# Kernel tuning notes

Measured on AMD Instinct MI355X. Metric: run time of the kernel, lower is better.

The kernel has to match this reference:

```python
import jax, jax.numpy as jnp
import numpy as np

HEAD_NUM = 8
QKV_DIM = 16
EMB = 128
SQRT_EMB = 11.313708498984761  # sqrt(128)
LOGIT_CLIP = 10.0


def _heads(x):
    # (B, n, H*d) -> (B, H, n, d)
    B, n, _ = x.shape
    return x.reshape(B, n, HEAD_NUM, QKV_DIM).transpose(0, 2, 1, 3)


def _mha(q, k, v, rank3_ninf_mask):
    # q: (B,H,n,d), k/v: (B,H,m,d), mask: (B,n,m)
    score = jnp.einsum('bhnd,bhmd->bhnm', q, k) / jnp.sqrt(jnp.float32(QKV_DIM))
    score = score + rank3_ninf_mask[:, None, :, :]
    w = jax.nn.softmax(score, axis=3)
    out = jnp.einsum('bhnm,bhmd->bhnd', w, v)
    B, H, n, d = out.shape
    return out.transpose(0, 2, 1, 3).reshape(B, n, H * d)


def setup_inputs() -> dict:
    key = jax.random.key(0)
    ks = jax.random.split(key, 20)
    B, N, P = 32, 512, 512
    s = 1.0 / np.sqrt(EMB)
    inp = {
        'encoded_nodes': jax.random.normal(ks[0], (B, N, EMB), jnp.float32),
        'encoded_graph': jax.random.normal(ks[1], (B, N, EMB), jnp.float32),
        'encoded_q1': jax.random.normal(ks[2], (B, P, EMB), jnp.float32),
        'encoded_first_graph': jax.random.normal(ks[3], (B, P, EMB), jnp.float32),
        'encoded_last_node': jax.random.normal(ks[4], (B, P, EMB), jnp.float32),
        'encoded_last_graph': jax.random.normal(ks[5], (B, P, EMB), jnp.float32),
        'ninf_mask': jnp.zeros((B, P, N), jnp.float32),
        # weights stored (in, out); torch Linear y = x @ W.T
        'Wq_first': jax.random.uniform(ks[6], (EMB, EMB), jnp.float32, -s, s),
        'Wq_last': jax.random.uniform(ks[7], (EMB, EMB), jnp.float32, -s, s),
        'Wk': jax.random.uniform(ks[8], (EMB, EMB), jnp.float32, -s, s),
        'Wv': jax.random.uniform(ks[9], (EMB, EMB), jnp.float32, -s, s),
        'Wq_first_e': jax.random.uniform(ks[10], (EMB, EMB), jnp.float32, -s, s),
        'Wq_last_e': jax.random.uniform(ks[11], (EMB, EMB), jnp.float32, -s, s),
        'Wk_e': jax.random.uniform(ks[12], (EMB, EMB), jnp.float32, -s, s),
        'Wv_e': jax.random.uniform(ks[13], (EMB, EMB), jnp.float32, -s, s),
        'Wcomb1': jax.random.uniform(ks[14], (EMB, EMB), jnp.float32, -s, s),
        'bcomb1': jax.random.uniform(ks[15], (EMB,), jnp.float32, -s, s),
        'Wcomb2': jax.random.uniform(ks[16], (EMB, EMB), jnp.float32, -s, s),
        'bcomb2': jax.random.uniform(ks[17], (EMB,), jnp.float32, -s, s),
    }
    return inp


def reference(encoded_nodes, encoded_graph, encoded_q1, encoded_first_graph,
              encoded_last_node, encoded_last_graph, ninf_mask,
              Wq_first, Wq_last, Wk, Wv,
              Wq_first_e, Wq_last_e, Wk_e, Wv_e,
              Wcomb1, bcomb1, Wcomb2, bcomb2):
    # set_kv
    k = _heads(encoded_nodes @ Wk)
    v = _heads(encoded_nodes @ Wv)
    k_e = _heads(encoded_graph @ Wk_e)
    v_e = _heads(encoded_graph @ Wv_e)
    # set_q1
    q_first = _heads(encoded_q1 @ Wq_first)
    q_first_e = _heads(encoded_first_graph @ Wq_first_e)
    # forward
    q_last = _heads(encoded_last_node @ Wq_last)
    q_last_e = _heads(encoded_last_graph @ Wq_last_e)
    q = (q_first + q_last) + (q_first_e + q_last_e)
    out1 = _mha(q, k, v, ninf_mask)
    out2 = _mha(q, k_e, v_e, ninf_mask)
    mh_out = (out1 @ Wcomb1 + bcomb1) + (out2 @ Wcomb2 + bcomb2)
    # single-head scoring against summed keys: (B,n,e) x (B,N,e) -> (B,n,N)
    shk = encoded_nodes + encoded_graph
    score = jnp.einsum('bne,bNe->bnN', mh_out, shk) / SQRT_EMB
    score = LOGIT_CLIP * jnp.tanh(score) + ninf_mask
    probs = jax.nn.softmax(score, axis=2)
    return probs
```

## Files before the change

### kernel.cpp

```cpp
#include <hip/hip_runtime.h>

#define BATCH 32
#define SEQ   512
#define EMBD  128
#define HEADS 8
#define HD    16
#define ROWS  (BATCH*SEQ)
#define TILE_R 64
#define NTILES (ROWS/TILE_R)

__device__ __forceinline__ void gemm_tile(const float* __restrict__ A,
                                          const float* __restrict__ W,
                                          int rowBase, int tid,
                                          float* sA, float* sW,
                                          float acc[8][4])
{
    __syncthreads();
    {
        const float4* Ag = (const float4*)(A + (size_t)rowBase * EMBD);
        const float4* Wg = (const float4*)W;
        float4* sA4 = (float4*)sA;
        float4* sW4 = (float4*)sW;
        #pragma unroll
        for (int k = 0; k < 8; ++k)  sA4[tid + k*256] = Ag[tid + k*256];
        #pragma unroll
        for (int k = 0; k < 16; ++k) sW4[tid + k*256] = Wg[tid + k*256];
    }
    __syncthreads();
    const int r0 = (tid >> 5) * 8;
    const int c0 = (tid & 31) * 4;
    for (int e0 = 0; e0 < EMBD; e0 += 4) {
        float a[8][4];
        #pragma unroll
        for (int r = 0; r < 8; ++r)
            *(float4*)&a[r][0] = *(const float4*)&sA[(r0+r)*EMBD + e0];
        float w[4][4];
        #pragma unroll
        for (int j = 0; j < 4; ++j)
            *(float4*)&w[j][0] = *(const float4*)&sW[(e0+j)*EMBD + c0];
        #pragma unroll
        for (int r = 0; r < 8; ++r) {
            #pragma unroll
            for (int c = 0; c < 4; ++c)
                acc[r][c] += a[r][0]*w[0][c] + a[r][1]*w[1][c]
                           + a[r][2]*w[2][c] + a[r][3]*w[3][c];
        }
    }
}

__device__ __forceinline__ void store_tile(float* __restrict__ out,
                                           int rowBase, int tid,
                                           float acc[8][4])
{
    const int r0 = (tid >> 5) * 8;
    const int c0 = (tid & 31) * 4;
    #pragma unroll
    for (int r = 0; r < 8; ++r)
        *(float4*)(out + (size_t)(rowBase + r0 + r)*EMBD + c0) =
            make_float4(acc[r][0], acc[r][1], acc[r][2], acc[r][3]);
}

__global__ __launch_bounds__(256) void proj_q_kernel(
    const float* __restrict__ A0, const float* __restrict__ W0,
    const float* __restrict__ A1, const float* __restrict__ W1,
    const float* __restrict__ A2, const float* __restrict__ W2,
    const float* __restrict__ A3, const float* __restrict__ W3,
    float* __restrict__ out)
{
    extern __shared__ float smem[];
    float* sA = smem;
    float* sW = smem + TILE_R*EMBD;
    const int tid = threadIdx.x;
    const int rowBase = blockIdx.x * TILE_R;
    float acc[8][4];
    #pragma unroll
    for (int r = 0; r < 8; ++r)
        #pragma unroll
        for (int c = 0; c < 4; ++c) acc[r][c] = 0.f;
    gemm_tile(A0, W0, rowBase, tid, sA, sW, acc);
    gemm_tile(A1, W1, rowBase, tid, sA, sW, acc);
    gemm_tile(A2, W2, rowBase, tid, sA, sW, acc);
    gemm_tile(A3, W3, rowBase, tid, sA, sW, acc);
    store_tile(out, rowBase, tid, acc);
}

__global__ __launch_bounds__(256) void proj_kv_kernel(
    const float* __restrict__ nodes, const float* __restrict__ graph,
    const float* __restrict__ Wk,  const float* __restrict__ Wv,
    const float* __restrict__ Wke, const float* __restrict__ Wve,
    float* __restrict__ Kb, float* __restrict__ Vb,
    float* __restrict__ Keb, float* __restrict__ Veb)
{
    extern __shared__ float smem[];
    float* sA = smem;
    float* sW = smem + TILE_R*EMBD;
    const int tid = threadIdx.x;
    const int rowBase = blockIdx.x * TILE_R;
    const int job = blockIdx.y;
    const float* A = (job < 2) ? nodes : graph;
    const float* W = (job == 0) ? Wk : (job == 1) ? Wv : (job == 2) ? Wke : Wve;
    float* out    = (job == 0) ? Kb : (job == 1) ? Vb : (job == 2) ? Keb : Veb;
    float acc[8][4];
    #pragma unroll
    for (int r = 0; r < 8; ++r)
        #pragma unroll
        for (int c = 0; c < 4; ++c) acc[r][c] = 0.f;
    gemm_tile(A, W, rowBase, tid, sA, sW, acc);
    store_tile(out, rowBase, tid, acc);
}

__global__ __launch_bounds__(256) void combine_kernel(
    const float* __restrict__ A0, const float* __restrict__ W0,
    const float* __restrict__ A1, const float* __restrict__ W1,
    const float* __restrict__ b0, const float* __restrict__ b1,
    float* __restrict__ out)
{
    extern __shared__ float smem[];
    float* sA = smem;
    float* sW = smem + TILE_R*EMBD;
    const int tid = threadIdx.x;
    const int rowBase = blockIdx.x * TILE_R;
    const int c0 = (tid & 31) * 4;
    float bv[4];
    #pragma unroll
    for (int c = 0; c < 4; ++c) bv[c] = b0[c0+c] + b1[c0+c];
    float acc[8][4];
    #pragma unroll
    for (int r = 0; r < 8; ++r)
        #pragma unroll
        for (int c = 0; c < 4; ++c) acc[r][c] = bv[c];
    gemm_tile(A0, W0, rowBase, tid, sA, sW, acc);
    gemm_tile(A1, W1, rowBase, tid, sA, sW, acc);
    store_tile(out, rowBase, tid, acc);
}

__global__ __launch_bounds__(512) void attn_kernel(
    const float* __restrict__ Qm, const float* __restrict__ Km,
    const float* __restrict__ Vm, const float* __restrict__ Kem,
    const float* __restrict__ Vem, const float* __restrict__ mask,
    float* __restrict__ out1, float* __restrict__ out2)
{
    extern __shared__ float smem[];
    float4* sK  = (float4*)smem;
    float4* sV  = sK  + 2048;
    float4* sKe = sV  + 2048;
    float4* sVe = sKe + 2048;
    const int tid = threadIdx.x;
    const int b = blockIdx.x >> 3;
    const int h = blockIdx.x & 7;
    const int base4 = b*(SEQ*EMBD/4) + h*(HD/4);
    {
        const float4* K4  = (const float4*)Km;
        const float4* V4  = (const float4*)Vm;
        const float4* Ke4 = (const float4*)Kem;
        const float4* Ve4 = (const float4*)Vem;
        #pragma unroll
        for (int k = 0; k < 4; ++k) {
            int i = tid + k*512;
            int m = i >> 2, j = i & 3;
            int g = base4 + m*(EMBD/4) + j;
            sK[i]  = K4[g];
            sV[i]  = V4[g];
            sKe[i] = Ke4[g];
            sVe[i] = Ve4[g];
        }
    }
    __syncthreads();

    const int row = tid;
    float q[16];
    {
        const float4* Q4 = (const float4*)Qm;
        #pragma unroll
        for (int j = 0; j < 4; ++j)
            *(float4*)&q[j*4] = Q4[base4 + row*(EMBD/4) + j];
    }
    const float* mrow = mask + ((size_t)b*SEQ + row)*SEQ;

    float l1 = 0.f, l2 = 0.f;
    float acc1[16], acc2[16];
    #pragma unroll
    for (int d = 0; d < 16; ++d) { acc1[d] = 0.f; acc2[d] = 0.f; }

    for (int m = 0; m < SEQ; ++m) {
        const float mk = mrow[m];
        {
            float4 k0 = sK[m*4+0], k1 = sK[m*4+1], k2 = sK[m*4+2], k3 = sK[m*4+3];
            float s = q[0]*k0.x + q[1]*k0.y + q[2]*k0.z + q[3]*k0.w
                    + q[4]*k1.x + q[5]*k1.y + q[6]*k1.z + q[7]*k1.w
                    + q[8]*k2.x + q[9]*k2.y + q[10]*k2.z + q[11]*k2.w
                    + q[12]*k3.x + q[13]*k3.y + q[14]*k3.z + q[15]*k3.w;
            float p = __expf(s*0.25f + mk);
            l1 += p;
            float4 v0 = sV[m*4+0], v1 = sV[m*4+1], v2 = sV[m*4+2], v3 = sV[m*4+3];
            acc1[0]+=p*v0.x;  acc1[1]+=p*v0.y;  acc1[2]+=p*v0.z;  acc1[3]+=p*v0.w;
            acc1[4]+=p*v1.x;  acc1[5]+=p*v1.y;  acc1[6]+=p*v1.z;  acc1[7]+=p*v1.w;
            acc1[8]+=p*v2.x;  acc1[9]+=p*v2.y;  acc1[10]+=p*v2.z; acc1[11]+=p*v2.w;
            acc1[12]+=p*v3.x; acc1[13]+=p*v3.y; acc1[14]+=p*v3.z; acc1[15]+=p*v3.w;
        }
        {
            float4 k0 = sKe[m*4+0], k1 = sKe[m*4+1], k2 = sKe[m*4+2], k3 = sKe[m*4+3];
            float s = q[0]*k0.x + q[1]*k0.y + q[2]*k0.z + q[3]*k0.w
                    + q[4]*k1.x + q[5]*k1.y + q[6]*k1.z + q[7]*k1.w
                    + q[8]*k2.x + q[9]*k2.y + q[10]*k2.z + q[11]*k2.w
                    + q[12]*k3.x + q[13]*k3.y + q[14]*k3.z + q[15]*k3.w;
            float p = __expf(s*0.25f + mk);
            l2 += p;
            float4 v0 = sVe[m*4+0], v1 = sVe[m*4+1], v2 = sVe[m*4+2], v3 = sVe[m*4+3];
            acc2[0]+=p*v0.x;  acc2[1]+=p*v0.y;  acc2[2]+=p*v0.z;  acc2[3]+=p*v0.w;
            acc2[4]+=p*v1.x;  acc2[5]+=p*v1.y;  acc2[6]+=p*v1.z;  acc2[7]+=p*v1.w;
            acc2[8]+=p*v2.x;  acc2[9]+=p*v2.y;  acc2[10]+=p*v2.z; acc2[11]+=p*v2.w;
            acc2[12]+=p*v3.x; acc2[13]+=p*v3.y; acc2[14]+=p*v3.z; acc2[15]+=p*v3.w;
        }
    }
    const float inv1 = 1.f / l1;
    const float inv2 = 1.f / l2;
    float4* o14 = (float4*)out1;
    float4* o24 = (float4*)out2;
    #pragma unroll
    for (int j = 0; j < 4; ++j) {
        o14[base4 + row*(EMBD/4) + j] = make_float4(acc1[j*4]*inv1, acc1[j*4+1]*inv1,
                                                    acc1[j*4+2]*inv1, acc1[j*4+3]*inv1);
        o24[base4 + row*(EMBD/4) + j] = make_float4(acc2[j*4]*inv2, acc2[j*4+1]*inv2,
                                                    acc2[j*4+2]*inv2, acc2[j*4+3]*inv2);
    }
}

#define RB 16
#define MT 128
__global__ __launch_bounds__(256) void final_kernel(
    const float* __restrict__ mh, const float* __restrict__ nodes,
    const float* __restrict__ graph, const float* __restrict__ mask,
    float* __restrict__ out)
{
    extern __shared__ float smem[];
    float*  sShk = smem;
    float*  sMh  = smem + MT*EMBD;
    float*  sS   = sMh + RB*EMBD;
    float*  sInv = sS + RB*SEQ;
    float4* sShk4 = (float4*)sShk;
    const int tid  = threadIdx.x;
    const int b    = blockIdx.x >> 5;
    const int row0 = (blockIdx.x & 31) * RB;

    {
        const float4* mh4 = (const float4*)(mh + ((size_t)b*SEQ + row0)*EMBD);
        ((float4*)sMh)[tid]       = mh4[tid];
        ((float4*)sMh)[tid + 256] = mh4[tid + 256];
    }

    const int mg = tid & 63;
    const int rg = tid >> 6;
    const float4* n4 = (const float4*)nodes;
    const float4* g4 = (const float4*)graph;

    for (int mt = 0; mt < SEQ/MT; ++mt) {
        const int m0 = mt * MT;
        __syncthreads();
        {
            const int gb = (b*SEQ + m0) * (EMBD/4);
            #pragma unroll
            for (int k = 0; k < 16; ++k) {
                int i = tid + k*256;
                int m = i >> 5, f = i & 31;
                float4 x = n4[gb + m*32 + f];
                float4 y = g4[gb + m*32 + f];
                float4 s4;
                s4.x = x.x + y.x; s4.y = x.y + y.y;
                s4.z = x.z + y.z; s4.w = x.w + y.w;
                sShk4[(m << 5) | (f ^ (m & 31))] = s4;
            }
        }
        __syncthreads();

        float acc[4][2];
        #pragma unroll
        for (int r = 0; r < 4; ++r) { acc[r][0] = 0.f; acc[r][1] = 0.f; }
        const int mA = mg*2, mB = mg*2 + 1;
        for (int e0 = 0; e0 < EMBD; e0 += 4) {
            const int f = e0 >> 2;
            float a[4][4];
            #pragma unroll
            for (int r = 0; r < 4; ++r)
                *(float4*)&a[r][0] = *(const float4*)&sMh[(rg*4+r)*EMBD + e0];
            float s0[4], s1[4];
            *(float4*)&s0[0] = sShk4[(mA << 5) | (f ^ (mA & 31))];
            *(float4*)&s1[0] = sShk4[(mB << 5) | (f ^ (mB & 31))];
            #pragma unroll
            for (int r = 0; r < 4; ++r) {
                acc[r][0] += a[r][0]*s0[0] + a[r][1]*s0[1] + a[r][2]*s0[2] + a[r][3]*s0[3];
                acc[r][1] += a[r][0]*s1[0] + a[r][1]*s1[1] + a[r][2]*s1[2] + a[r][3]*s1[3];
            }
        }
        #pragma unroll
        for (int r = 0; r < 4; ++r) {
            const int rr = rg*4 + r;
            const size_t mbase = ((size_t)b*SEQ + row0 + rr) * SEQ;
            #pragma unroll
            for (int mm = 0; mm < 2; ++mm) {
                const int m = m0 + mg*2 + mm;
                float sc = 10.f * tanhf(acc[r][mm] * 0.088388347648318447f)
                         + mask[mbase + m];
                sS[rr*SEQ + m] = sc;
            }
        }
    }
    __syncthreads();

    {
        const int r = tid >> 4, g = tid & 15;
        float sum = 0.f;
        for (int k = g; k < SEQ; k += 16) {
            float p = __expf(sS[r*SEQ + k]);
            sS[r*SEQ + k] = p;
            sum += p;
        }
        #pragma unroll
        for (int off = 8; off >= 1; off >>= 1) sum += __shfl_xor(sum, off, 16);
        if (g == 0) sInv[r] = 1.f / sum;
    }
    __syncthreads();

    float* orow = out + ((size_t)b*SEQ + row0) * SEQ;
    #pragma unroll
    for (int k = 0; k < 32; ++k) {
        int i = tid + k*256;
        int r = i >> 9;
        orow[i] = sS[i] * sInv[r];
    }
}

extern "C" void kernel_launch(void* const* d_in, const int* in_sizes, int n_in,
                              void* d_out, int out_size, void* d_ws, size_t ws_size,
                              hipStream_t stream)
{
    const float* nodes = (const float*)d_in[0];
    const float* graph = (const float*)d_in[1];
    const float* q1    = (const float*)d_in[2];
    const float* fg    = (const float*)d_in[3];
    const float* ln    = (const float*)d_in[4];
    const float* lg    = (const float*)d_in[5];
    const float* mask  = (const float*)d_in[6];
    const float* Wqf   = (const float*)d_in[7];
    const float* Wql   = (const float*)d_in[8];
    const float* Wk    = (const float*)d_in[9];
    const float* Wv    = (const float*)d_in[10];
    const float* Wqfe  = (const float*)d_in[11];
    const float* Wqle  = (const float*)d_in[12];
    const float* Wke   = (const float*)d_in[13];
    const float* Wve   = (const float*)d_in[14];
    const float* Wc1   = (const float*)d_in[15];
    const float* bc1   = (const float*)d_in[16];
    const float* Wc2   = (const float*)d_in[17];
    const float* bc2   = (const float*)d_in[18];

    float* ws = (float*)d_ws;
    const size_t BUF = (size_t)ROWS * EMBD;
    float* Qb  = ws;
    float* Kb  = ws + BUF;
    float* Vb  = ws + 2*BUF;
    float* Keb = ws + 3*BUF;
    float* Veb = ws + 4*BUF;
    float* mhb = Qb;
    float* o1  = (float*)d_out;
    float* o2  = o1 + BUF;

    const int LDS_GEMM  = (TILE_R*EMBD + EMBD*EMBD) * 4;
    const int LDS_ATTN  = 4 * SEQ * HD * 4;
    const int LDS_FINAL = (MT*EMBD + RB*EMBD + RB*SEQ + 16) * 4;
    hipFuncSetAttribute((const void*)proj_q_kernel,  hipFuncAttributeMaxDynamicSharedMemorySize, LDS_GEMM);
    hipFuncSetAttribute((const void*)proj_kv_kernel, hipFuncAttributeMaxDynamicSharedMemorySize, LDS_GEMM);
    hipFuncSetAttribute((const void*)combine_kernel, hipFuncAttributeMaxDynamicSharedMemorySize, LDS_GEMM);
    hipFuncSetAttribute((const void*)attn_kernel,    hipFuncAttributeMaxDynamicSharedMemorySize, LDS_ATTN);
    hipFuncSetAttribute((const void*)final_kernel,   hipFuncAttributeMaxDynamicSharedMemorySize, LDS_FINAL);

    proj_q_kernel<<<NTILES, 256, LDS_GEMM, stream>>>(
        q1, Wqf, ln, Wql, fg, Wqfe, lg, Wqle, Qb);
    proj_kv_kernel<<<dim3(NTILES, 4), 256, LDS_GEMM, stream>>>(
        nodes, graph, Wk, Wv, Wke, Wve, Kb, Vb, Keb, Veb);
    attn_kernel<<<BATCH*HEADS, 512, LDS_ATTN, stream>>>(
        Qb, Kb, Vb, Keb, Veb, mask, o1, o2);
    combine_kernel<<<NTILES, 256, LDS_GEMM, stream>>>(
        o1, Wc1, o2, Wc2, bc1, bc2, mhb);
    final_kernel<<<BATCH*32, 256, LDS_FINAL, stream>>>(
        mhb, nodes, graph, mask, (float*)d_out);
}
```

Baseline: 683.4 us.

## Drop LDS from projection GEMMs, merge projections, re-split attention and final softmax

Merges the Q and KV projection launches into one kernel and makes the projection and combine GEMMs read operands straight from global/cache instead of staging them in LDS, using smaller 32-row tiles. The attention kernel is reorganised so each 1024-thread block handles two heads of one K/V type instead of one head with both types, with vectorised mask loads. The final kernel keeps probabilities in registers with a wave-level row reduction instead of an LDS score buffer, and computes tanh through exp. The aim is more parallelism and fewer LDS round-trips and barriers, at the cost of more redundant global reads of weights and activations.

After: 653.3 us. 1.05x faster.

```diff
diff --git a/kernel.cpp b/kernel.cpp
--- a/kernel.cpp
+++ b/kernel.cpp
@@ -6,107 +6,86 @@
 #define HEADS 8
 #define HD    16
 #define ROWS  (BATCH*SEQ)
-#define TILE_R 64
-#define NTILES (ROWS/TILE_R)
-
-__device__ __forceinline__ void gemm_tile(const float* __restrict__ A,
-                                          const float* __restrict__ W,
-                                          int rowBase, int tid,
-                                          float* sA, float* sW,
-                                          float acc[8][4])
-{
-    __syncthreads();
-    {
-        const float4* Ag = (const float4*)(A + (size_t)rowBase * EMBD);
-        const float4* Wg = (const float4*)W;
-        float4* sA4 = (float4*)sA;
-        float4* sW4 = (float4*)sW;
-        #pragma unroll
-        for (int k = 0; k < 8; ++k)  sA4[tid + k*256] = Ag[tid + k*256];
-        #pragma unroll
-        for (int k = 0; k < 16; ++k) sW4[tid + k*256] = Wg[tid + k*256];
-    }
-    __syncthreads();
-    const int r0 = (tid >> 5) * 8;
+#define GR    32
+#define NT32  (ROWS/GR)
+
+__device__ __forceinline__ void gemm_nolds(const float* __restrict__ A,
+                                           const float* __restrict__ W,
+                                           int rowBase, int tid,
+                                           float acc[4][4])
+{
+    const int r0 = (tid >> 5) * 4;
     const int c0 = (tid & 31) * 4;
+    const float* Ab = A + (size_t)(rowBase + r0) * EMBD;
     for (int e0 = 0; e0 < EMBD; e0 += 4) {
-        float a[8][4];
-        #pragma unroll
-        for (int r = 0; r < 8; ++r)
-            *(float4*)&a[r][0] = *(const float4*)&sA[(r0+r)*EMBD + e0];
-        float w[4][4];
+        float4 a[4];
+        #pragma unroll
+        for (int r = 0; r < 4; ++r)
+            a[r] = *(const float4*)(Ab + r*EMBD + e0);
+        float4 w[4];
         #pragma unroll
         for (int j = 0; j < 4; ++j)
-            *(float4*)&w[j][0] = *(const float4*)&sW[(e0+j)*EMBD + c0];
-        #pragma unroll
-        for (int r = 0; r < 8; ++r) {
-            #pragma unroll
-            for (int c = 0; c < 4; ++c)
-                acc[r][c] += a[r][0]*w[0][c] + a[r][1]*w[1][c]
-                           + a[r][2]*w[2][c] + a[r][3]*w[3][c];
-        }
-    }
-}
-
-__device__ __forceinline__ void store_tile(float* __restrict__ out,
-                                           int rowBase, int tid,
-                                           float acc[8][4])
-{
-    const int r0 = (tid >> 5) * 8;
+            w[j] = *(const float4*)(W + (e0+j)*EMBD + c0);
+        #pragma unroll
+        for (int r = 0; r < 4; ++r) {
+            acc[r][0] += a[r].x*w[0].x + a[r].y*w[1].x + a[r].z*w[2].x + a[r].w*w[3].x;
+            acc[r][1] += a[r].x*w[0].y + a[r].y*w[1].y + a[r].z*w[2].y + a[r].w*w[3].y;
+            acc[r][2] += a[r].x*w[0].z + a[r].y*w[1].z + a[r].z*w[2].z + a[r].w*w[3].z;
+            acc[r][3] += a[r].x*w[0].w + a[r].y*w[1].w + a[r].z*w[2].w + a[r].w*w[3].w;
+        }
+    }
+}
+
+__device__ __forceinline__ void store_nolds(float* __restrict__ out,
+                                            int rowBase, int tid,
+                                            float acc[4][4])
+{
+    const int r0 = (tid >> 5) * 4;
     const int c0 = (tid & 31) * 4;
     #pragma unroll
-    for (int r = 0; r < 8; ++r)
+    for (int r = 0; r < 4; ++r)
         *(float4*)(out + (size_t)(rowBase + r0 + r)*EMBD + c0) =
             make_float4(acc[r][0], acc[r][1], acc[r][2], acc[r][3]);
 }
 
-__global__ __launch_bounds__(256) void proj_q_kernel(
-    const float* __restrict__ A0, const float* __restrict__ W0,
-    const float* __restrict__ A1, const float* __restrict__ W1,
-    const float* __restrict__ A2, const float* __restrict__ W2,
-    const float* __restrict__ A3, const float* __restrict__ W3,
-    float* __restrict__ out)
-{
-    extern __shared__ float smem[];
-    float* sA = smem;
-    float* sW = smem + TILE_R*EMBD;
+__global__ __launch_bounds__(256) void proj_all_kernel(
+    const float* __restrict__ nodes, const float* __restrict__ graph,
+    const float* __restrict__ q1,    const float* __restrict__ fg,
+    const float* __restrict__ ln,    const float* __restrict__ lg,
+    const float* __restrict__ Wqf,  const float* __restrict__ Wql,
+    const float* __restrict__ Wqfe, const float* __restrict__ Wqle,
+    const float* __restrict__ Wk,   const float* __restrict__ Wv,
+    const float* __restrict__ Wke,  const float* __restrict__ Wve,
+    float* __restrict__ Qb, float* __restrict__ Kb, float* __restrict__ Vb,
+    float* __restrict__ Keb, float* __restrict__ Veb)
+{
     const int tid = threadIdx.x;
-    const int rowBase = blockIdx.x * TILE_R;
-    float acc[8][4];
-    #pragma unroll
-    for (int r = 0; r < 8; ++r)
+    const int rowBase = blockIdx.x * GR;
+    const int job = blockIdx.y;
+    float acc[4][4];
+    #pragma unroll
+    for (int r = 0; r < 4; ++r)
         #pragma unroll
         for (int c = 0; c < 4; ++c) acc[r][c] = 0.f;
-    gemm_tile(A0, W0, rowBase, tid, sA, sW, acc);
-    gemm_tile(A1, W1, rowBase, tid, sA, sW, acc);
-    gemm_tile(A2, W2, rowBase, tid, sA, sW, acc);
-    gemm_tile(A3, W3, rowBase, tid, sA, sW, acc);
-    store_tile(out, rowBase, tid, acc);
-}
-
-__global__ __launch_bounds__(256) void proj_kv_kernel(
-    const float* __restrict__ nodes, const float* __restrict__ graph,
-    const float* __restrict__ Wk,  const float* __restrict__ Wv,
-    const float* __restrict__ Wke, const float* __restrict__ Wve,
-    float* __restrict__ Kb, float* __restrict__ Vb,
-    float* __restrict__ Keb, float* __restrict__ Veb)
-{
-    extern __shared__ float smem[];
-    float* sA = smem;
-    float* sW = smem + TILE_R*EMBD;
-    const int tid = threadIdx.x;
-    const int rowBase = blockIdx.x * TILE_R;
-    const int job = blockIdx.y;
-    const float* A = (job < 2) ? nodes : graph;
-    const float* W = (job == 0) ? Wk : (job == 1) ? Wv : (job == 2) ? Wke : Wve;
-    float* out    = (job == 0) ? Kb : (job == 1) ? Vb : (job == 2) ? Keb : Veb;
-    float acc[8][4];
-    #pragma unroll
-    for (int r = 0; r < 8; ++r)
-        #pragma unroll
-        for (int c = 0; c < 4; ++c) acc[r][c] = 0.f;
-    gemm_tile(A, W, rowBase, tid, sA, sW, acc);
-    store_tile(out, rowBase, tid, acc);
+    if (job == 0) {
+        gemm_nolds(q1, Wqf,  rowBase, tid, acc);
+        gemm_nolds(ln, Wql,  rowBase, tid, acc);
+        gemm_nolds(fg, Wqfe, rowBase, tid, acc);
+        gemm_nolds(lg, Wqle, rowBase, tid, acc);
+        store_nolds(Qb, rowBase, tid, acc);
+    } else if (job == 1) {
+        gemm_nolds(nodes, Wk, rowBase, tid, acc);
+        store_nolds(Kb, rowBase, tid, acc);
+    } else if (job == 2) {
+        gemm_nolds(nodes, Wv, rowBase, tid, acc);
+        store_nolds(Vb, rowBase, tid, acc);
+    } else if (job == 3) {
+        gemm_nolds(graph, Wke, rowBase, tid, acc);
+        store_nolds(Keb, rowBase, tid, acc);
+    } else {
+        gemm_nolds(graph, Wve, rowBase, tid, acc);
+        store_nolds(Veb, rowBase, tid, acc);
+    }
 }
 
 __global__ __launch_bounds__(256) void combine_kernel(
@@ -115,153 +94,142 @@
     const float* __restrict__ b0, const float* __restrict__ b1,
     float* __restrict__ out)
 {
-    extern __shared__ float smem[];
-    float* sA = smem;
-    float* sW = smem + TILE_R*EMBD;
     const int tid = threadIdx.x;
-    const int rowBase = blockIdx.x * TILE_R;
+    const int rowBase = blockIdx.x * GR;
     const int c0 = (tid & 31) * 4;
-    float bv[4];
-    #pragma unroll
-    for (int c = 0; c < 4; ++c) bv[c] = b0[c0+c] + b1[c0+c];
-    float acc[8][4];
-    #pragma unroll
-    for (int r = 0; r < 8; ++r)
-        #pragma unroll
-        for (int c = 0; c < 4; ++c) acc[r][c] = bv[c];
-    gemm_tile(A0, W0, rowBase, tid, sA, sW, acc);
-    gemm_tile(A1, W1, rowBase, tid, sA, sW, acc);
-    store_tile(out, rowBase, tid, acc);
-}
-
-__global__ __launch_bounds__(512) void attn_kernel(
+    float acc[4][4];
+    #pragma unroll
+    for (int c = 0; c < 4; ++c) {
+        float bv = b0[c0+c] + b1[c0+c];
+        #pragma unroll
+        for (int r = 0; r < 4; ++r) acc[r][c] = bv;
+    }
+    gemm_nolds(A0, W0, rowBase, tid, acc);
+    gemm_nolds(A1, W1, rowBase, tid, acc);
+    store_nolds(out, rowBase, tid, acc);
+}
+
+__global__ __launch_bounds__(1024) void attn_kernel(
     const float* __restrict__ Qm, const float* __restrict__ Km,
     const float* __restrict__ Vm, const float* __restrict__ Kem,
     const float* __restrict__ Vem, const float* __restrict__ mask,
     float* __restrict__ out1, float* __restrict__ out2)
 {
     extern __shared__ float smem[];
-    float4* sK  = (float4*)smem;
-    float4* sV  = sK  + 2048;
-    float4* sKe = sV  + 2048;
-    float4* sVe = sKe + 2048;
-    const int tid = threadIdx.x;
-    const int b = blockIdx.x >> 3;
-    const int h = blockIdx.x & 7;
-    const int base4 = b*(SEQ*EMBD/4) + h*(HD/4);
+    float4* sK0 = (float4*)smem;
+    float4* sV0 = sK0 + 2048;
+    float4* sK1 = sV0 + 2048;
+    float4* sV1 = sK1 + 2048;
+    const int tid  = threadIdx.x;
+    const int type = blockIdx.x & 1;
+    const int hp   = (blockIdx.x >> 1) & 3;
+    const int b    = blockIdx.x >> 3;
+    const float* K = type ? Kem : Km;
+    const float* V = type ? Vem : Vm;
+    float* outp    = type ? out2 : out1;
+    const int h0 = hp * 2;
     {
-        const float4* K4  = (const float4*)Km;
-        const float4* V4  = (const float4*)Vm;
-        const float4* Ke4 = (const float4*)Kem;
-        const float4* Ve4 = (const float4*)Vem;
-        #pragma unroll
-        for (int k = 0; k < 4; ++k) {
-            int i = tid + k*512;
+        const float4* K4 = (const float4*)K;
+        const float4* V4 = (const float4*)V;
+        const int b0 = b*(SEQ*EMBD/4) + h0*(HD/4);
+        #pragma unroll
+        for (int k = 0; k < 2; ++k) {
+            int i = tid + k*1024;
             int m = i >> 2, j = i & 3;
-            int g = base4 + m*(EMBD/4) + j;
-            sK[i]  = K4[g];
-            sV[i]  = V4[g];
-            sKe[i] = Ke4[g];
-            sVe[i] = Ve4[g];
+            int g0 = b0 + m*(EMBD/4) + j;
+            sK0[i] = K4[g0];
+            sV0[i] = V4[g0];
+            sK1[i] = K4[g0 + 4];
+            sV1[i] = V4[g0 + 4];
         }
     }
     __syncthreads();
 
-    const int row = tid;
+    const int head = tid >> 9;
+    const int row  = tid & 511;
+    const float4* sK = head ? sK1 : sK0;
+    const float4* sV = head ? sV1 : sV0;
+
     float q[16];
     {
         const float4* Q4 = (const float4*)Qm;
+        const int qb = b*(SEQ*EMBD/4) + row*(EMBD/4) + (h0+head)*(HD/4);
         #pragma unroll
         for (int j = 0; j < 4; ++j)
-            *(float4*)&q[j*4] = Q4[base4 + row*(EMBD/4) + j];
-    }
-    const float* mrow = mask + ((size_t)b*SEQ + row)*SEQ;
-
-    float l1 = 0.f, l2 = 0.f;
-    float acc1[16], acc2[16];
-    #pragma unroll
-    for (int d = 0; d < 16; ++d) { acc1[d] = 0.f; acc2[d] = 0.f; }
-
-    for (int m = 0; m < SEQ; ++m) {
-        const float mk = mrow[m];
-        {
+            *(float4*)&q[j*4] = Q4[qb + j];
+    }
+    const float4* mrow4 = (const float4*)(mask + ((size_t)b*SEQ + row)*SEQ);
+
+    float l = 0.f;
+    float acc[16];
+    #pragma unroll
+    for (int d = 0; d < 16; ++d) acc[d] = 0.f;
+
+    for (int m4 = 0; m4 < SEQ/4; ++m4) {
+        float4 mk4 = mrow4[m4];
+        float mkv[4] = {mk4.x, mk4.y, mk4.z, mk4.w};
+        #pragma unroll
+        for (int u = 0; u < 4; ++u) {
+            const int m = m4*4 + u;
             float4 k0 = sK[m*4+0], k1 = sK[m*4+1], k2 = sK[m*4+2], k3 = sK[m*4+3];
             float s = q[0]*k0.x + q[1]*k0.y + q[2]*k0.z + q[3]*k0.w
                     + q[4]*k1.x + q[5]*k1.y + q[6]*k1.z + q[7]*k1.w
                     + q[8]*k2.x + q[9]*k2.y + q[10]*k2.z + q[11]*k2.w
                     + q[12]*k3.x + q[13]*k3.y + q[14]*k3.z + q[15]*k3.w;
-            float p = __expf(s*0.25f + mk);
-            l1 += p;
+            float p = __expf(s*0.25f + mkv[u]);
+            l += p;
             float4 v0 = sV[m*4+0], v1 = sV[m*4+1], v2 = sV[m*4+2], v3 = sV[m*4+3];
-            acc1[0]+=p*v0.x;  acc1[1]+=p*v0.y;  acc1[2]+=p*v0.z;  acc1[3]+=p*v0.w;
-            acc1[4]+=p*v1.x;  acc1[5]+=p*v1.y;  acc1[6]+=p*v1.z;  acc1[7]+=p*v1.w;
-            acc1[8]+=p*v2.x;  acc1[9]+=p*v2.y;  acc1[10]+=p*v2.z; acc1[11]+=p*v2.w;
-            acc1[12]+=p*v3.x; acc1[13]+=p*v3.y; acc1[14]+=p*v3.z; acc1[15]+=p*v3.w;
-        }
-        {
-            float4 k0 = sKe[m*4+0], k1 = sKe[m*4+1], k2 = sKe[m*4+2], k3 = sKe[m*4+3];
-            float s = q[0]*k0.x + q[1]*k0.y + q[2]*k0.z + q[3]*k0.w
-                    + q[4]*k1.x + q[5]*k1.y + q[6]*k1.z + q[7]*k1.w
-                    + q[8]*k2.x + q[9]*k2.y + q[10]*k2.z + q[11]*k2.w
-                    + q[12]*k3.x + q[13]*k3.y + q[14]*k3.z + q[15]*k3.w;
-            float p = __expf(s*0.25f + mk);
-            l2 += p;
-            float4 v0 = sVe[m*4+0], v1 = sVe[m*4+1], v2 = sVe[m*4+2], v3 = sVe[m*4+3];
-            acc2[0]+=p*v0.x;  acc2[1]+=p*v0.y;  acc2[2]+=p*v0.z;  acc2[3]+=p*v0.w;
-            acc2[4]+=p*v1.x;  acc2[5]+=p*v1.y;  acc2[6]+=p*v1.z;  acc2[7]+=p*v1.w;
-            acc2[8]+=p*v2.x;  acc2[9]+=p*v2.y;  acc2[10]+=p*v2.z; acc2[11]+=p*v2.w;
-            acc2[12]+=p*v3.x; acc2[13]+=p*v3.y; acc2[14]+=p*v3.z; acc2[15]+=p*v3.w;
-        }
-    }
-    const float inv1 = 1.f / l1;
-    const float inv2 = 1.f / l2;
-    float4* o14 = (float4*)out1;
-    float4* o24 = (float4*)out2;
-    #pragma unroll
-    for (int j = 0; j < 4; ++j) {
-        o14[base4 + row*(EMBD/4) + j] = make_float4(acc1[j*4]*inv1, acc1[j*4+1]*inv1,
-                                                    acc1[j*4+2]*inv1, acc1[j*4+3]*inv1);
-        o24[base4 + row*(EMBD/4) + j] = make_float4(acc2[j*4]*inv2, acc2[j*4+1]*inv2,
-                                                    acc2[j*4+2]*inv2, acc2[j*4+3]*inv2);
-    }
-}
-
-#define RB 16
-#define MT 128
-__global__ __launch_bounds__(256) void final_kernel(
+            acc[0]+=p*v0.x;  acc[1]+=p*v0.y;  acc[2]+=p*v0.z;  acc[3]+=p*v0.w;
+            acc[4]+=p*v1.x;  acc[5]+=p*v1.y;  acc[6]+=p*v1.z;  acc[7]+=p*v1.w;
+            acc[8]+=p*v2.x;  acc[9]+=p*v2.y;  acc[10]+=p*v2.z; acc[11]+=p*v2.w;
+            acc[12]+=p*v3.x; acc[13]+=p*v3.y; acc[14]+=p*v3.z; acc[15]+=p*v3.w;
+        }
+    }
+    const float inv = 1.f / l;
+    float4* o4 = (float4*)outp;
+    const int ob = b*(SEQ*EMBD/4) + row*(EMBD/4) + (h0+head)*(HD/4);
+    #pragma unroll
+    for (int j = 0; j < 4; ++j)
+        o4[ob + j] = make_float4(acc[j*4]*inv, acc[j*4+1]*inv,
+                                 acc[j*4+2]*inv, acc[j*4+3]*inv);
+}
+
+#define RB 32
+#define MT 64
+__global__ __launch_bounds__(512) void final_kernel(
     const float* __restrict__ mh, const float* __restrict__ nodes,
     const float* __restrict__ graph, const float* __restrict__ mask,
     float* __restrict__ out)
 {
     extern __shared__ float smem[];
-    float*  sShk = smem;
-    float*  sMh  = smem + MT*EMBD;
-    float*  sS   = sMh + RB*EMBD;
-    float*  sInv = sS + RB*SEQ;
-    float4* sShk4 = (float4*)sShk;
+    float4* sShk4 = (float4*)smem;
+    float*  sMh   = smem + MT*EMBD;
     const int tid  = threadIdx.x;
-    const int b    = blockIdx.x >> 5;
-    const int row0 = (blockIdx.x & 31) * RB;
+    const int b    = blockIdx.x >> 4;
+    const int row0 = (blockIdx.x & 15) * RB;
+    const int mg = tid & 63;
+    const int rg = tid >> 6;
 
     {
         const float4* mh4 = (const float4*)(mh + ((size_t)b*SEQ + row0)*EMBD);
         ((float4*)sMh)[tid]       = mh4[tid];
-        ((float4*)sMh)[tid + 256] = mh4[tid + 256];
-    }
-
-    const int mg = tid & 63;
-    const int rg = tid >> 6;
+        ((float4*)sMh)[tid + 512] = mh4[tid + 512];
+    }
+
     const float4* n4 = (const float4*)nodes;
     const float4* g4 = (const float4*)graph;
-
+    float p[4][8];
+    float rs[4] = {0.f, 0.f, 0.f, 0.f};
+
+    #pragma unroll
     for (int mt = 0; mt < SEQ/MT; ++mt) {
         const int m0 = mt * MT;
         __syncthreads();
         {
             const int gb = (b*SEQ + m0) * (EMBD/4);
             #pragma unroll
-            for (int k = 0; k < 16; ++k) {
-                int i = tid + k*256;
+            for (int k = 0; k < 4; ++k) {
+                int i = tid + k*512;
                 int m = i >> 5, f = i & 31;
                 float4 x = n4[gb + m*32 + f];
                 float4 y = g4[gb + m*32 + f];
@@ -273,60 +241,45 @@
         }
         __syncthreads();
 
-        float acc[4][2];
-        #pragma unroll
-        for (int r = 0; r < 4; ++r) { acc[r][0] = 0.f; acc[r][1] = 0.f; }
-        const int mA = mg*2, mB = mg*2 + 1;
+        float acc[4] = {0.f, 0.f, 0.f, 0.f};
+        const int m = mg;
+        #pragma unroll 8
         for (int e0 = 0; e0 < EMBD; e0 += 4) {
             const int f = e0 >> 2;
-            float a[4][4];
-            #pragma unroll
-            for (int r = 0; r < 4; ++r)
-                *(float4*)&a[r][0] = *(const float4*)&sMh[(rg*4+r)*EMBD + e0];
-            float s0[4], s1[4];
-            *(float4*)&s0[0] = sShk4[(mA << 5) | (f ^ (mA & 31))];
-            *(float4*)&s1[0] = sShk4[(mB << 5) | (f ^ (mB & 31))];
+            float4 s = sShk4[(m << 5) | (f ^ (m & 31))];
             #pragma unroll
             for (int r = 0; r < 4; ++r) {
-                acc[r][0] += a[r][0]*s0[0] + a[r][1]*s0[1] + a[r][2]*s0[2] + a[r][3]*s0[3];
-                acc[r][1] += a[r][0]*s1[0] + a[r][1]*s1[1] + a[r][2]*s1[2] + a[r][3]*s1[3];
+                const float* a = &sMh[(rg*4+r)*EMBD + e0];
+                acc[r] += a[0]*s.x + a[1]*s.y + a[2]*s.z + a[3]*s.w;
             }
         }
         #pragma unroll
         for (int r = 0; r < 4; ++r) {
-            const int rr = rg*4 + r;
-            const size_t mbase = ((size_t)b*SEQ + row0 + rr) * SEQ;
-            #pragma unroll
-            for (int mm = 0; mm < 2; ++mm) {
-                const int m = m0 + mg*2 + mm;
-                float sc = 10.f * tanhf(acc[r][mm] * 0.088388347648318447f)
-                         + mask[mbase + m];
-                sS[rr*SEQ + m] = sc;
-            }
-        }
-    }
-    __syncthreads();
-
-    {
-        const int r = tid >> 4, g = tid & 15;
-        float sum = 0.f;
-        for (int k = g; k < SEQ; k += 16) {
-            float p = __expf(sS[r*SEQ + k]);
-            sS[r*SEQ + k] = p;
-            sum += p;
-        }
-        #pragma unroll
-        for (int off = 8; off >= 1; off >>= 1) sum += __shfl_xor(sum, off, 16);
-        if (g == 0) sInv[r] = 1.f / sum;
-    }
-    __syncthreads();
-
-    float* orow = out + ((size_t)b*SEQ + row0) * SEQ;
-    #pragma unroll
-    for (int k = 0; k < 32; ++k) {
-        int i = tid + k*256;
-        int r = i >> 9;
-        orow[i] = sS[i] * sInv[r];
+            const int row = row0 + rg*4 + r;
+            float x = acc[r] * 0.088388347648318447f;
+            float t = 1.f - 2.f / (__expf(2.f*x) + 1.f);
+            float sc = 10.f*t + mask[((size_t)b*SEQ + row)*SEQ + m0 + mg];
+            float pp = __expf(sc);
+            p[r][mt] = pp;
+            rs[r] += pp;
+        }
+    }
+
+    #pragma unroll
+    for (int r = 0; r < 4; ++r) {
+        float s = rs[r];
+        #pragma unroll
+        for (int off = 32; off >= 1; off >>= 1) s += __shfl_xor(s, off);
+        rs[r] = 1.f / s;
+    }
+
+    #pragma unroll
+    for (int mt = 0; mt < SEQ/MT; ++mt) {
+        #pragma unroll
+        for (int r = 0; r < 4; ++r) {
+            const int row = row0 + rg*4 + r;
+            out[((size_t)b*SEQ + row)*SEQ + mt*MT + mg] = p[r][mt] * rs[r];
+        }
     }
 }
 
@@ -365,23 +318,19 @@
     float* o1  = (float*)d_out;
     float* o2  = o1 + BUF;
 
-    const int LDS_GEMM  = (TILE_R*EMBD + EMBD*EMBD) * 4;
     const int LDS_ATTN  = 4 * SEQ * HD * 4;
-    const int LDS_FINAL = (MT*EMBD + RB*EMBD + RB*SEQ + 16) * 4;
-    hipFuncSetAttribute((const void*)proj_q_kernel,  hipFuncAttributeMaxDynamicSharedMemorySize, LDS_GEMM);
-    hipFuncSetAttribute((const void*)proj_kv_kernel, hipFuncAttributeMaxDynamicSharedMemorySize, LDS_GEMM);
-    hipFuncSetAttribute((const void*)combine_kernel, hipFuncAttributeMaxDynamicSharedMemorySize, LDS_GEMM);
-    hipFuncSetAttribute((const void*)attn_kernel,    hipFuncAttributeMaxDynamicSharedMemorySize, LDS_ATTN);
-    hipFuncSetAttribute((const void*)final_kernel,   hipFuncAttributeMaxDynamicSharedMemorySize, LDS_FINAL);
-
-    proj_q_kernel<<<NTILES, 256, LDS_GEMM, stream>>>(
-        q1, Wqf, ln, Wql, fg, Wqfe, lg, Wqle, Qb);
-    proj_kv_kernel<<<dim3(NTILES, 4), 256, LDS_GEMM, stream>>>(
-        nodes, graph, Wk, Wv, Wke, Wve, Kb, Vb, Keb, Veb);
-    attn_kernel<<<BATCH*HEADS, 512, LDS_ATTN, stream>>>(
+    const int LDS_FINAL = (MT*EMBD + RB*EMBD) * 4;
+    hipFuncSetAttribute((const void*)attn_kernel,  hipFuncAttributeMaxDynamicSharedMemorySize, LDS_ATTN);
+    hipFuncSetAttribute((const void*)final_kernel, hipFuncAttributeMaxDynamicSharedMemorySize, LDS_FINAL);
+
+    proj_all_kernel<<<dim3(NT32, 5), 256, 0, stream>>>(
+        nodes, graph, q1, fg, ln, lg,
+        Wqf, Wql, Wqfe, Wqle, Wk, Wv, Wke, Wve,
+        Qb, Kb, Vb, Keb, Veb);
+    attn_kernel<<<BATCH*8, 1024, LDS_ATTN, stream>>>(
         Qb, Kb, Vb, Keb, Veb, mask, o1, o2);
-    combine_kernel<<<NTILES, 256, LDS_GEMM, stream>>>(
+    combine_kernel<<<NT32, 256, 0, stream>>>(
         o1, Wc1, o2, Wc2, bc1, bc2, mhb);
-    final_kernel<<<BATCH*32, 256, LDS_FINAL, stream>>>(
+    final_kernel<<<BATCH*(SEQ/RB), 512, LDS_FINAL, stream>>>(
         mhb, nodes, graph, mask, (float*)d_out);
 }
```
